# Kernel tuning notes

Measured on AMD Instinct MI355X. Metric: run time of the kernel, lower is better.

The kernel has to match this reference:

```python
import jax, jax.numpy as jnp
import numpy as np

N = 100000
E = 3200000
IN_C = 128
HID = 128


def setup_inputs() -> dict:
    key = jax.random.key(0)
    k1, k2, k3, k4, k5 = jax.random.split(key, 5)
    x = jax.random.normal(k1, (N, IN_C), dtype=jnp.float32)
    edge_index = jax.random.randint(k2, (2, E), 0, N, dtype=jnp.int64)
    edge_weight = jax.random.uniform(k3, (E,), dtype=jnp.float32)
    # GCNConv linear weight [out, in] (applied as x @ W.T), glorot-ish scale
    W = jax.random.normal(k4, (HID, IN_C), dtype=jnp.float32) / np.sqrt(IN_C)
    bias = jnp.zeros((HID,), dtype=jnp.float32)
    # PReLU per-channel alpha, torch default init 0.25
    alpha = jnp.full((HID,), 0.25, dtype=jnp.float32)
    return {"x": x, "edge_index": edge_index, "edge_weight": edge_weight,
            "W": W, "bias": bias, "alpha": alpha}


def reference(x, edge_index, edge_weight, W, bias, alpha):
    n = x.shape[0]
    # gcn_norm with self-loops (fill value 1.0)
    loop_idx = jnp.arange(n, dtype=edge_index.dtype)
    row = jnp.concatenate([edge_index[0], loop_idx])  # source
    col = jnp.concatenate([edge_index[1], loop_idx])  # target
    ew = jnp.concatenate([edge_weight, jnp.ones((n,), dtype=edge_weight.dtype)])
    deg = jax.ops.segment_sum(ew, col, num_segments=n)  # in-degree by weight
    dinv = jnp.where(deg > 0, jax.lax.rsqrt(deg), 0.0)
    norm = dinv[row] * ew * dinv[col]  # [E+N]
    # linear transform first (GCNConv order), then gather-scatter aggregation
    h = x @ W.T  # [N, HID]
    msgs = norm[:, None] * h[row]  # [E+N, HID]
    out = jax.ops.segment_sum(msgs, col, num_segments=n) + bias  # [N, HID]
    # PReLU with per-channel alpha
    return jnp.where(out > 0, out, alpha * out)
```

## Files before the change

### kernel.cpp

```cpp
#include <hip/hip_runtime.h>


#define NBLK    512
#define MAXBKT  1600
#define QSCALE  32767.0f

__device__ __forceinline__ unsigned bf16pack2(float a, float b) {
    unsigned ua = __float_as_uint(a);
    ua = (ua + 0x7fffu + ((ua >> 16) & 1u)) >> 16;
    unsigned ub = __float_as_uint(b);
    ub = (ub + 0x7fffu + ((ub >> 16) & 1u)) >> 16;
    return ua | (ub << 16);
}

__device__ __forceinline__ float2 bf16unpack2(unsigned u) {
    return make_float2(__uint_as_float(u << 16),
                       __uint_as_float(u & 0xffff0000u));
}

__global__ __launch_bounds__(256) void p1_hist(const int* __restrict__ col,
                                               unsigned* __restrict__ hist,
                                               int e, int nbkt, int epb) {
    __shared__ unsigned lh[MAXBKT];
    int b = blockIdx.x;
    for (int k = threadIdx.x; k < nbkt; k += 256) lh[k] = 0;
    __syncthreads();
    int s = b * epb, en = s + epb; if (en > e) en = e;
    for (int i = s + threadIdx.x; i < en; i += 256)
        atomicAdd(&lh[col[i] >> 6], 1u);
    __syncthreads();
    for (int k = threadIdx.x; k < nbkt; k += 256)
        hist[(size_t)k * NBLK + b] = lh[k];
}

__global__ __launch_bounds__(1024) void scan_partial2(
    const unsigned* __restrict__ a, unsigned* __restrict__ part, int m) {
    __shared__ unsigned red[1024];
    int t = threadIdx.x, i = blockIdx.x * 1024 + t;
    red[t] = (i < m) ? a[i] : 0;
    __syncthreads();
    #pragma unroll
    for (int d = 512; d > 0; d >>= 1) {
        if (t < d) red[t] += red[t + d];
        __syncthreads();
    }
    if (t == 0) part[blockIdx.x] = red[0];
}

__global__ __launch_bounds__(1024) void scan_base2(
    unsigned* __restrict__ part, int nb, int* __restrict__ offs, int n, int e) {
    __shared__ unsigned s[1024];
    int t = threadIdx.x;
    unsigned v = (t < nb) ? part[t] : 0;
    s[t] = v;
    __syncthreads();
    for (int d = 1; d < 1024; d <<= 1) {
        unsigned add = (t >= d) ? s[t - d] : 0;
        __syncthreads();
        s[t] += add;
        __syncthreads();
    }
    if (t < nb) part[t] = s[t] - v;
    if (t == 0) offs[n] = e;
}

__global__ __launch_bounds__(1024) void scan_write2(
    unsigned* __restrict__ a, const unsigned* __restrict__ part, int m) {
    __shared__ unsigned s[1024];
    int t = threadIdx.x, i = blockIdx.x * 1024 + t;
    unsigned v = (i < m) ? a[i] : 0;
    s[t] = v;
    __syncthreads();
    for (int d = 1; d < 1024; d <<= 1) {
        unsigned add = (t >= d) ? s[t - d] : 0;
        __syncthreads();
        s[t] += add;
        __syncthreads();
    }
    if (i < m) a[i] = part[blockIdx.x] + s[t] - v;
}

__global__ __launch_bounds__(256) void p2_scatter(
    const int* __restrict__ col, const int* __restrict__ row,
    const float* __restrict__ ew, const unsigned* __restrict__ base,
    unsigned long long* __restrict__ pay, int e, int nbkt, int epb) {
    __shared__ unsigned lbase[MAXBKT];
    __shared__ unsigned lcur[MAXBKT];
    int b = blockIdx.x;
    for (int k = threadIdx.x; k < nbkt; k += 256) {
        lbase[k] = base[(size_t)k * NBLK + b];
        lcur[k] = 0;
    }
    __syncthreads();
    int s = b * epb, en = s + epb; if (en > e) en = e;
    for (int i = s + threadIdx.x; i < en; i += 256) {
        int c = col[i];
        int bk = c >> 6;
        unsigned q  = (unsigned)(ew[i] * QSCALE + 0.5f);
        unsigned lo = ((unsigned)row[i] << 15) | q;
        unsigned rk = atomicAdd(&lcur[bk], 1u);
        pay[(size_t)lbase[bk] + rk] =
            ((unsigned long long)(unsigned)(c & 63) << 32) | lo;
    }
}

__global__ __launch_bounds__(256) void p3_build(
    const unsigned long long* __restrict__ pay,
    const unsigned* __restrict__ histBase,
    unsigned* __restrict__ csr, int* __restrict__ offs,
    float* __restrict__ dinv, int n, int nbkt, int e) {
    __shared__ unsigned cnt[64], wsum[64], lofs[64], cur[64];
    int bk = blockIdx.x;
    int zs = (int)histBase[(size_t)bk * NBLK];
    int ze = (bk + 1 < nbkt) ? (int)histBase[(size_t)(bk + 1) * NBLK] : e;
    int t = threadIdx.x;
    if (t < 64) { cnt[t] = 0; wsum[t] = 0; cur[t] = 0; }
    __syncthreads();
    for (int p = zs + t; p < ze; p += 256) {
        unsigned long long v = pay[p];
        int l = (int)(v >> 32) & 63;
        atomicAdd(&cnt[l], 1u);
        atomicAdd(&wsum[l], (unsigned)v & 0x7fffu);
    }
    __syncthreads();
    if (t == 0) {
        unsigned run = 0;
        for (int l = 0; l < 64; ++l) { lofs[l] = run; run += cnt[l]; }
    }
    __syncthreads();
    for (int p = zs + t; p < ze; p += 256) {
        unsigned long long v = pay[p];
        int l = (int)(v >> 32) & 63;
        unsigned rk = atomicAdd(&cur[l], 1u);
        csr[zs + lofs[l] + rk] = (unsigned)v;
    }
    if (t < 64) {
        int node = bk * 64 + t;
        if (node < n) {
            offs[node] = zs + (int)lofs[t];
            float dg = 1.0f + (float)wsum[t] * (1.0f / QSCALE);
            dinv[node] = rsqrtf(dg);
        }
    }
}

__global__ __launch_bounds__(256) void gemm_kernel(const float* __restrict__ x,
                                                   const float* __restrict__ W,
                                                   unsigned* __restrict__ h, int n) {
    __shared__ float Wt[128][128];
    int t = threadIdx.x;
    const float4* W4 = (const float4*)W;
    #pragma unroll
    for (int it = 0; it < 16; ++it) {
        int i = t + it * 256;
        float4 v = W4[i];
        int o  = i >> 5;
        int kb = (i & 31) << 2;
        Wt[kb + 0][o ^ (((kb + 0) & 7) << 2)] = v.x;
        Wt[kb + 1][o ^ (((kb + 1) & 7) << 2)] = v.y;
        Wt[kb + 2][o ^ (((kb + 2) & 7) << 2)] = v.z;
        Wt[kb + 3][o ^ (((kb + 3) & 7) << 2)] = v.w;
    }
    __syncthreads();

    int tc = t & 31;
    int rs = t >> 5;
    int r0 = blockIdx.x * 64 + rs * 8;
    if (r0 >= n) return;
    const float4* x4 = (const float4*)x;

    float acc[8][4];
    #pragma unroll
    for (int ri = 0; ri < 8; ++ri)
        #pragma unroll
        for (int j = 0; j < 4; ++j) acc[ri][j] = 0.0f;

    int rcnt = n - r0; if (rcnt > 8) rcnt = 8;

    if (rcnt == 8) {
        for (int kq = 0; kq < 32; ++kq) {
            int kb = kq << 2;
            float4 wv0 = *(const float4*)&Wt[kb + 0][(4 * tc) ^ (((kb + 0) & 7) << 2)];
            float4 wv1 = *(const float4*)&Wt[kb + 1][(4 * tc) ^ (((kb + 1) & 7) << 2)];
            float4 wv2 = *(const float4*)&Wt[kb + 2][(4 * tc) ^ (((kb + 2) & 7) << 2)];
            float4 wv3 = *(const float4*)&Wt[kb + 3][(4 * tc) ^ (((kb + 3) & 7) << 2)];
            #pragma unroll
            for (int ri = 0; ri < 8; ++ri) {
                float4 xv = x4[(size_t)(r0 + ri) * 32 + kq];
                acc[ri][0] += xv.x * wv0.x + xv.y * wv1.x + xv.z * wv2.x + xv.w * wv3.x;
                acc[ri][1] += xv.x * wv0.y + xv.y * wv1.y + xv.z * wv2.y + xv.w * wv3.y;
                acc[ri][2] += xv.x * wv0.z + xv.y * wv1.z + xv.z * wv2.z + xv.w * wv3.z;
                acc[ri][3] += xv.x * wv0.w + xv.y * wv1.w + xv.z * wv2.w + xv.w * wv3.w;
            }
        }
        uint2* h2 = (uint2*)h;
        #pragma unroll
        for (int ri = 0; ri < 8; ++ri)
            h2[(size_t)(r0 + ri) * 32 + tc] =
                make_uint2(bf16pack2(acc[ri][0], acc[ri][1]),
                           bf16pack2(acc[ri][2], acc[ri][3]));
    } else {
        for (int kq = 0; kq < 32; ++kq) {
            int kb = kq << 2;
            float4 wv0 = *(const float4*)&Wt[kb + 0][(4 * tc) ^ (((kb + 0) & 7) << 2)];
            float4 wv1 = *(const float4*)&Wt[kb + 1][(4 * tc) ^ (((kb + 1) & 7) << 2)];
            float4 wv2 = *(const float4*)&Wt[kb + 2][(4 * tc) ^ (((kb + 2) & 7) << 2)];
            float4 wv3 = *(const float4*)&Wt[kb + 3][(4 * tc) ^ (((kb + 3) & 7) << 2)];
            for (int ri = 0; ri < rcnt; ++ri) {
                float4 xv = x4[(size_t)(r0 + ri) * 32 + kq];
                acc[ri][0] += xv.x * wv0.x + xv.y * wv1.x + xv.z * wv2.x + xv.w * wv3.x;
                acc[ri][1] += xv.x * wv0.y + xv.y * wv1.y + xv.z * wv2.y + xv.w * wv3.y;
                acc[ri][2] += xv.x * wv0.z + xv.y * wv1.z + xv.z * wv2.z + xv.w * wv3.z;
                acc[ri][3] += xv.x * wv0.w + xv.y * wv1.w + xv.z * wv2.w + xv.w * wv3.w;
            }
        }
        uint2* h2 = (uint2*)h;
        for (int ri = 0; ri < rcnt; ++ri)
            h2[(size_t)(r0 + ri) * 32 + tc] =
                make_uint2(bf16pack2(acc[ri][0], acc[ri][1]),
                           bf16pack2(acc[ri][2], acc[ri][3]));
    }
}

__global__ __launch_bounds__(256) void aggregate_kernel(
    const unsigned* __restrict__ h, const unsigned* __restrict__ csr,
    const int* __restrict__ offs, const float* __restrict__ dinv,
    const float* __restrict__ bias, const float* __restrict__ alpha,
    float* __restrict__ out, int n) {
    int w = (blockIdx.x * 256 + threadIdx.x) >> 6;
    if (w >= n) return;
    int lane = threadIdx.x & 63;

    int beg = offs[w], end = offs[w + 1];
    float ax = 0.0f, ay = 0.0f;

    int i = beg;
    int end4 = beg + ((end - beg) & ~3);
    for (; i < end4; i += 4) {
        unsigned p0 = csr[i],     p1 = csr[i + 1];
        unsigned p2 = csr[i + 2], p3 = csr[i + 3];
        unsigned s0 = p0 >> 15, s1 = p1 >> 15, s2 = p2 >> 15, s3 = p3 >> 15;
        float d0 = dinv[s0], d1 = dinv[s1], d2 = dinv[s2], d3 = dinv[s3];
        float2 v0 = bf16unpack2(h[(size_t)s0 * 64 + lane]);
        float2 v1 = bf16unpack2(h[(size_t)s1 * 64 + lane]);
        float2 v2 = bf16unpack2(h[(size_t)s2 * 64 + lane]);
        float2 v3 = bf16unpack2(h[(size_t)s3 * 64 + lane]);
        float a0 = d0 * (float)(p0 & 0x7fffu) * (1.0f / QSCALE);
        float a1 = d1 * (float)(p1 & 0x7fffu) * (1.0f / QSCALE);
        float a2 = d2 * (float)(p2 & 0x7fffu) * (1.0f / QSCALE);
        float a3 = d3 * (float)(p3 & 0x7fffu) * (1.0f / QSCALE);
        ax += a0 * v0.x; ay += a0 * v0.y;
        ax += a1 * v1.x; ay += a1 * v1.y;
        ax += a2 * v2.x; ay += a2 * v2.y;
        ax += a3 * v3.x; ay += a3 * v3.y;
    }
    for (; i < end; ++i) {
        unsigned p = csr[i];
        unsigned s = p >> 15;
        float a = dinv[s] * (float)(p & 0x7fffu) * (1.0f / QSCALE);
        float2 v = bf16unpack2(h[(size_t)s * 64 + lane]);
        ax += a * v.x; ay += a * v.y;
    }

    float dc = dinv[w];
    float2 hc = bf16unpack2(h[(size_t)w * 64 + lane]);
    ax += dc * hc.x; ay += dc * hc.y;

    float2 bv = ((const float2*)bias)[lane];
    float2 av = ((const float2*)alpha)[lane];
    float ox = ax * dc + bv.x;
    float oy = ay * dc + bv.y;
    ox = ox > 0.0f ? ox : av.x * ox;
    oy = oy > 0.0f ? oy : av.y * oy;
    ((float2*)out)[(size_t)w * 64 + lane] = make_float2(ox, oy);
}

extern "C" void kernel_launch(void* const* d_in, const int* in_sizes, int n_in,
                              void* d_out, int out_size, void* d_ws, size_t ws_size,
                              hipStream_t stream) {
    const float* x     = (const float*)d_in[0];
    const int*   ei    = (const int*)d_in[1];
    const float* ew    = (const float*)d_in[2];
    const float* W     = (const float*)d_in[3];
    const float* bias  = (const float*)d_in[4];
    const float* alpha = (const float*)d_in[5];
    float* out = (float*)d_out;

    const int n = in_sizes[0] / 128;
    const int e = in_sizes[1] / 2;
    const int* row = ei;
    const int* col = ei + e;

    const int nbkt = (n + 63) >> 6;
    const int m    = nbkt * NBLK;
    const int epb  = (e + NBLK - 1) / NBLK;
    const int nb2  = (m + 1023) / 1024;

    char* ws = (char*)d_ws;
    size_t off = 0;
    auto alloc = [&](size_t bytes) -> char* {
        char* p = ws + off;
        off = (off + bytes + 255) & ~(size_t)255;
        return p;
    };
    unsigned*           hist = (unsigned*)          alloc((size_t)m * 4);
    unsigned*           part = (unsigned*)          alloc((size_t)1024 * 4);
    int*                offs = (int*)               alloc((size_t)(n + 1) * 4);
    float*              dinv = (float*)             alloc((size_t)n * 4);
    unsigned long long* pay  = (unsigned long long*)alloc((size_t)e * 8);
    unsigned*           csr  = (unsigned*)          alloc((size_t)e * 4);
    unsigned*           h    = (unsigned*)          alloc((size_t)n * 128 * 2);
    (void)ws_size; (void)n_in; (void)out_size;

    p1_hist<<<NBLK, 256, 0, stream>>>(col, hist, e, nbkt, epb);
    scan_partial2<<<nb2, 1024, 0, stream>>>(hist, part, m);
    scan_base2<<<1, 1024, 0, stream>>>(part, nb2, offs, n, e);
    scan_write2<<<nb2, 1024, 0, stream>>>(hist, part, m);
    p2_scatter<<<NBLK, 256, 0, stream>>>(col, row, ew, hist, pay, e, nbkt, epb);
    p3_build<<<nbkt, 256, 0, stream>>>(pay, hist, csr, offs, dinv, n, nbkt, e);

    int gg = (n + 63) / 64;
    gemm_kernel<<<gg, 256, 0, stream>>>(x, W, h, n);

    int ga = (n + 3) / 4;
    aggregate_kernel<<<ga, 256, 0, stream>>>(h, csr, offs, dinv, bias, alpha, out, n);
}
```

Baseline: 295.5 us.

## Precompute per-edge coefficients and swizzle aggregate block order across XCDs

Adds an af_fill kernel that computes each edge's normalized coefficient (dinv[src] times the dequantized weight) once into a float array, so the aggregate loop no longer performs a dependent random dinv gather per edge. The aggregate kernel also reads its row offsets through readfirstlane to keep them scalar, and remaps block IDs so consecutive node groups land on the same XCD when the grid is divisible by 8. The cost is an extra kernel launch plus a write and read of 4 bytes per edge. The swizzle only takes effect when the block count is a multiple of 8, which holds for n=100000.

```diff
diff --git a/kernel.cpp b/kernel.cpp
--- a/kernel.cpp
+++ b/kernel.cpp
@@ -141,6 +141,16 @@
             float dg = 1.0f + (float)wsum[t] * (1.0f / QSCALE);
             dinv[node] = rsqrtf(dg);
         }
+    }
+}
+
+__global__ __launch_bounds__(256) void af_fill(const unsigned* __restrict__ csr,
+                                               const float* __restrict__ dinv,
+                                               float* __restrict__ af, int e) {
+    int i = blockIdx.x * 256 + threadIdx.x;
+    if (i < e) {
+        unsigned v = csr[i];
+        af[i] = dinv[v >> 15] * ((float)(v & 0x7fffu) * (1.0f / QSCALE));
     }
 }
 
@@ -224,40 +234,40 @@
 
 __global__ __launch_bounds__(256) void aggregate_kernel(
     const unsigned* __restrict__ h, const unsigned* __restrict__ csr,
-    const int* __restrict__ offs, const float* __restrict__ dinv,
-    const float* __restrict__ bias, const float* __restrict__ alpha,
-    float* __restrict__ out, int n) {
-    int w = (blockIdx.x * 256 + threadIdx.x) >> 6;
+    const float* __restrict__ af, const int* __restrict__ offs,
+    const float* __restrict__ dinv, const float* __restrict__ bias,
+    const float* __restrict__ alpha, float* __restrict__ out, int n, int swzq) {
+    int bid = blockIdx.x;
+    int sb  = swzq ? ((bid & 7) * swzq + (bid >> 3)) : bid;
+    int w = sb * 4 + (threadIdx.x >> 6);
     if (w >= n) return;
     int lane = threadIdx.x & 63;
 
-    int beg = offs[w], end = offs[w + 1];
+    int beg = __builtin_amdgcn_readfirstlane(offs[w]);
+    int end = __builtin_amdgcn_readfirstlane(offs[w + 1]);
     float ax = 0.0f, ay = 0.0f;
 
     int i = beg;
     int end4 = beg + ((end - beg) & ~3);
     for (; i < end4; i += 4) {
-        unsigned p0 = csr[i],     p1 = csr[i + 1];
-        unsigned p2 = csr[i + 2], p3 = csr[i + 3];
-        unsigned s0 = p0 >> 15, s1 = p1 >> 15, s2 = p2 >> 15, s3 = p3 >> 15;
-        float d0 = dinv[s0], d1 = dinv[s1], d2 = dinv[s2], d3 = dinv[s3];
-        float2 v0 = bf16unpack2(h[(size_t)s0 * 64 + lane]);
-        float2 v1 = bf16unpack2(h[(size_t)s1 * 64 + lane]);
-        float2 v2 = bf16unpack2(h[(size_t)s2 * 64 + lane]);
-        float2 v3 = bf16unpack2(h[(size_t)s3 * 64 + lane]);
-        float a0 = d0 * (float)(p0 & 0x7fffu) * (1.0f / QSCALE);
-        float a1 = d1 * (float)(p1 & 0x7fffu) * (1.0f / QSCALE);
-        float a2 = d2 * (float)(p2 & 0x7fffu) * (1.0f / QSCALE);
-        float a3 = d3 * (float)(p3 & 0x7fffu) * (1.0f / QSCALE);
+        unsigned s0 = csr[i]     >> 15, s1 = csr[i + 1] >> 15;
+        unsigned s2 = csr[i + 2] >> 15, s3 = csr[i + 3] >> 15;
+        float a0 = af[i],     a1 = af[i + 1];
+        float a2 = af[i + 2], a3 = af[i + 3];
+        unsigned u0 = h[(size_t)s0 * 64 + lane];
+        unsigned u1 = h[(size_t)s1 * 64 + lane];
+        unsigned u2 = h[(size_t)s2 * 64 + lane];
+        unsigned u3 = h[(size_t)s3 * 64 + lane];
+        float2 v0 = bf16unpack2(u0), v1 = bf16unpack2(u1);
+        float2 v2 = bf16unpack2(u2), v3 = bf16unpack2(u3);
         ax += a0 * v0.x; ay += a0 * v0.y;
         ax += a1 * v1.x; ay += a1 * v1.y;
         ax += a2 * v2.x; ay += a2 * v2.y;
         ax += a3 * v3.x; ay += a3 * v3.y;
     }
     for (; i < end; ++i) {
-        unsigned p = csr[i];
-        unsigned s = p >> 15;
-        float a = dinv[s] * (float)(p & 0x7fffu) * (1.0f / QSCALE);
+        unsigned s = csr[i] >> 15;
+        float a = af[i];
         float2 v = bf16unpack2(h[(size_t)s * 64 + lane]);
         ax += a * v.x; ay += a * v.y;
     }
@@ -309,6 +319,7 @@
     float*              dinv = (float*)             alloc((size_t)n * 4);
     unsigned long long* pay  = (unsigned long long*)alloc((size_t)e * 8);
     unsigned*           csr  = (unsigned*)          alloc((size_t)e * 4);
+    float*              afv  = (float*)             alloc((size_t)e * 4);
     unsigned*           h    = (unsigned*)          alloc((size_t)n * 128 * 2);
     (void)ws_size; (void)n_in; (void)out_size;
 
@@ -318,10 +329,13 @@
     scan_write2<<<nb2, 1024, 0, stream>>>(hist, part, m);
     p2_scatter<<<NBLK, 256, 0, stream>>>(col, row, ew, hist, pay, e, nbkt, epb);
     p3_build<<<nbkt, 256, 0, stream>>>(pay, hist, csr, offs, dinv, n, nbkt, e);
+    af_fill<<<(e + 255) / 256, 256, 0, stream>>>(csr, dinv, afv, e);
 
     int gg = (n + 63) / 64;
     gemm_kernel<<<gg, 256, 0, stream>>>(x, W, h, n);
 
     int ga = (n + 3) / 4;
-    aggregate_kernel<<<ga, 256, 0, stream>>>(h, csr, offs, dinv, bias, alpha, out, n);
-}
+    int swzq = (ga % 8 == 0) ? ga / 8 : 0;
+    aggregate_kernel<<<ga, 256, 0, stream>>>(h, csr, afv, offs, dinv,
+                                             bias, alpha, out, n, swzq);
+}
```

Measured after the change: 296.1 us. Within noise of the previous version (+0.2%).

## Tile hidden features into column slabs and prefold source dinv into CSR weights

Applied to the files above, without the earlier changes.

The GEMM now writes h in a tiled layout: 8 slabs of 16 channels per node, so each 32-byte slab row belongs to one node. Aggregation runs over a 2D grid of node by slab. Each wave processes 8 edges at once, with 8 lanes covering 16 channels, then combines the partial sums with xor shuffles. A new pass folds dinv[src] into the quantized 15-bit edge weight, which removes the per-edge dinv gather but adds requantization error and an extra pass over the edges. The intent is to shrink each slab's gather footprint so it stays in cache, at the cost of reading the CSR eight times and doing more, narrower gathers.

```diff
diff --git a/kernel.cpp b/kernel.cpp
--- a/kernel.cpp
+++ b/kernel.cpp
@@ -4,6 +4,9 @@
 #define NBLK    512
 #define MAXBKT  1600
 #define QSCALE  32767.0f
+#define NTILE   8
+
+typedef float vfloat2 __attribute__((ext_vector_type(2)));
 
 __device__ __forceinline__ unsigned bf16pack2(float a, float b) {
     unsigned ua = __float_as_uint(a);
@@ -144,9 +147,20 @@
     }
 }
 
+__global__ __launch_bounds__(256) void csr2_fill(const unsigned* __restrict__ csr,
+                                                 const float* __restrict__ dinv,
+                                                 unsigned* __restrict__ csr2, int e) {
+    int i = blockIdx.x * 256 + threadIdx.x;
+    if (i < e) {
+        unsigned v = csr[i];
+        float a = dinv[v >> 15] * ((float)(v & 0x7fffu) * (1.0f / QSCALE));
+        csr2[i] = (v & 0xffff8000u) | (unsigned)(a * QSCALE + 0.5f);
+    }
+}
+
 __global__ __launch_bounds__(256) void gemm_kernel(const float* __restrict__ x,
                                                    const float* __restrict__ W,
-                                                   unsigned* __restrict__ h, int n) {
+                                                   unsigned* __restrict__ ht, int n) {
     __shared__ float Wt[128][128];
     int t = threadIdx.x;
     const float4* W4 = (const float4*)W;
@@ -176,6 +190,9 @@
         for (int j = 0; j < 4; ++j) acc[ri][j] = 0.0f;
 
     int rcnt = n - r0; if (rcnt > 8) rcnt = 8;
+
+    uint2* h2 = (uint2*)ht;
+    size_t obase = (size_t)(tc >> 2) * n * 4 + (tc & 3);
 
     if (rcnt == 8) {
         for (int kq = 0; kq < 32; ++kq) {
@@ -193,10 +210,9 @@
                 acc[ri][3] += xv.x * wv0.w + xv.y * wv1.w + xv.z * wv2.w + xv.w * wv3.w;
             }
         }
-        uint2* h2 = (uint2*)h;
         #pragma unroll
         for (int ri = 0; ri < 8; ++ri)
-            h2[(size_t)(r0 + ri) * 32 + tc] =
+            h2[obase + (size_t)(r0 + ri) * 4] =
                 make_uint2(bf16pack2(acc[ri][0], acc[ri][1]),
                            bf16pack2(acc[ri][2], acc[ri][3]));
     } else {
@@ -214,65 +230,67 @@
                 acc[ri][3] += xv.x * wv0.w + xv.y * wv1.w + xv.z * wv2.w + xv.w * wv3.w;
             }
         }
-        uint2* h2 = (uint2*)h;
         for (int ri = 0; ri < rcnt; ++ri)
-            h2[(size_t)(r0 + ri) * 32 + tc] =
+            h2[obase + (size_t)(r0 + ri) * 4] =
                 make_uint2(bf16pack2(acc[ri][0], acc[ri][1]),
                            bf16pack2(acc[ri][2], acc[ri][3]));
     }
 }
 
 __global__ __launch_bounds__(256) void aggregate_kernel(
-    const unsigned* __restrict__ h, const unsigned* __restrict__ csr,
+    const unsigned* __restrict__ ht, const unsigned* __restrict__ csr2,
     const int* __restrict__ offs, const float* __restrict__ dinv,
     const float* __restrict__ bias, const float* __restrict__ alpha,
     float* __restrict__ out, int n) {
-    int w = (blockIdx.x * 256 + threadIdx.x) >> 6;
+    int tile = blockIdx.y;
+    int w = blockIdx.x * 4 + (threadIdx.x >> 6);
     if (w >= n) return;
     int lane = threadIdx.x & 63;
-
-    int beg = offs[w], end = offs[w + 1];
+    int g = lane >> 3, c2 = lane & 7;
+    const unsigned* slab = ht + (size_t)tile * n * 8;
+
+    int beg = __builtin_amdgcn_readfirstlane(offs[w]);
+    int end = __builtin_amdgcn_readfirstlane(offs[w + 1]);
+
     float ax = 0.0f, ay = 0.0f;
-
-    int i = beg;
-    int end4 = beg + ((end - beg) & ~3);
-    for (; i < end4; i += 4) {
-        unsigned p0 = csr[i],     p1 = csr[i + 1];
-        unsigned p2 = csr[i + 2], p3 = csr[i + 3];
-        unsigned s0 = p0 >> 15, s1 = p1 >> 15, s2 = p2 >> 15, s3 = p3 >> 15;
-        float d0 = dinv[s0], d1 = dinv[s1], d2 = dinv[s2], d3 = dinv[s3];
-        float2 v0 = bf16unpack2(h[(size_t)s0 * 64 + lane]);
-        float2 v1 = bf16unpack2(h[(size_t)s1 * 64 + lane]);
-        float2 v2 = bf16unpack2(h[(size_t)s2 * 64 + lane]);
-        float2 v3 = bf16unpack2(h[(size_t)s3 * 64 + lane]);
-        float a0 = d0 * (float)(p0 & 0x7fffu) * (1.0f / QSCALE);
-        float a1 = d1 * (float)(p1 & 0x7fffu) * (1.0f / QSCALE);
-        float a2 = d2 * (float)(p2 & 0x7fffu) * (1.0f / QSCALE);
-        float a3 = d3 * (float)(p3 & 0x7fffu) * (1.0f / QSCALE);
-        ax += a0 * v0.x; ay += a0 * v0.y;
-        ax += a1 * v1.x; ay += a1 * v1.y;
-        ax += a2 * v2.x; ay += a2 * v2.y;
-        ax += a3 * v3.x; ay += a3 * v3.y;
-    }
-    for (; i < end; ++i) {
-        unsigned p = csr[i];
-        unsigned s = p >> 15;
-        float a = dinv[s] * (float)(p & 0x7fffu) * (1.0f / QSCALE);
-        float2 v = bf16unpack2(h[(size_t)s * 64 + lane]);
-        ax += a * v.x; ay += a * v.y;
-    }
-
-    float dc = dinv[w];
-    float2 hc = bf16unpack2(h[(size_t)w * 64 + lane]);
-    ax += dc * hc.x; ay += dc * hc.y;
-
-    float2 bv = ((const float2*)bias)[lane];
-    float2 av = ((const float2*)alpha)[lane];
-    float ox = ax * dc + bv.x;
-    float oy = ay * dc + bv.y;
-    ox = ox > 0.0f ? ox : av.x * ox;
-    oy = oy > 0.0f ? oy : av.y * oy;
-    ((float2*)out)[(size_t)w * 64 + lane] = make_float2(ox, oy);
+    int i = beg + g;
+    for (; i + 8 < end; i += 16) {
+        unsigned v0 = __builtin_nontemporal_load(&csr2[i]);
+        unsigned v1 = __builtin_nontemporal_load(&csr2[i + 8]);
+        unsigned u0 = slab[(size_t)(v0 >> 15) * 8 + c2];
+        unsigned u1 = slab[(size_t)(v1 >> 15) * 8 + c2];
+        float a0 = (float)(v0 & 0x7fffu) * (1.0f / QSCALE);
+        float a1 = (float)(v1 & 0x7fffu) * (1.0f / QSCALE);
+        float2 h0 = bf16unpack2(u0), h1 = bf16unpack2(u1);
+        ax += a0 * h0.x; ay += a0 * h0.y;
+        ax += a1 * h1.x; ay += a1 * h1.y;
+    }
+    if (i < end) {
+        unsigned v = __builtin_nontemporal_load(&csr2[i]);
+        unsigned u = slab[(size_t)(v >> 15) * 8 + c2];
+        float a = (float)(v & 0x7fffu) * (1.0f / QSCALE);
+        float2 hv = bf16unpack2(u);
+        ax += a * hv.x; ay += a * hv.y;
+    }
+
+    ax += __shfl_xor(ax, 8);  ay += __shfl_xor(ay, 8);
+    ax += __shfl_xor(ax, 16); ay += __shfl_xor(ay, 16);
+    ax += __shfl_xor(ax, 32); ay += __shfl_xor(ay, 32);
+
+    if (lane < 8) {
+        float dc = dinv[w];
+        float2 hw = bf16unpack2(slab[(size_t)w * 8 + lane]);
+        ax += dc * hw.x; ay += dc * hw.y;
+        float2 bv = ((const float2*)bias)[tile * 8 + lane];
+        float2 av = ((const float2*)alpha)[tile * 8 + lane];
+        float ox = ax * dc + bv.x;
+        float oy = ay * dc + bv.y;
+        ox = ox > 0.0f ? ox : av.x * ox;
+        oy = oy > 0.0f ? oy : av.y * oy;
+        vfloat2 ov; ov.x = ox; ov.y = oy;
+        __builtin_nontemporal_store(ov,
+            (vfloat2*)&((float2*)out)[(size_t)w * 64 + tile * 8 + lane]);
+    }
 }
 
 extern "C" void kernel_launch(void* const* d_in, const int* in_sizes, int n_in,
@@ -309,7 +327,8 @@
     float*              dinv = (float*)             alloc((size_t)n * 4);
     unsigned long long* pay  = (unsigned long long*)alloc((size_t)e * 8);
     unsigned*           csr  = (unsigned*)          alloc((size_t)e * 4);
-    unsigned*           h    = (unsigned*)          alloc((size_t)n * 128 * 2);
+    unsigned*           csr2 = (unsigned*)          alloc((size_t)e * 4);
+    unsigned*           ht   = (unsigned*)          alloc((size_t)n * 128 * 2);
     (void)ws_size; (void)n_in; (void)out_size;
 
     p1_hist<<<NBLK, 256, 0, stream>>>(col, hist, e, nbkt, epb);
@@ -318,10 +337,13 @@
     scan_write2<<<nb2, 1024, 0, stream>>>(hist, part, m);
     p2_scatter<<<NBLK, 256, 0, stream>>>(col, row, ew, hist, pay, e, nbkt, epb);
     p3_build<<<nbkt, 256, 0, stream>>>(pay, hist, csr, offs, dinv, n, nbkt, e);
+    csr2_fill<<<(e + 255) / 256, 256, 0, stream>>>(csr, dinv, csr2, e);
 
     int gg = (n + 63) / 64;
-    gemm_kernel<<<gg, 256, 0, stream>>>(x, W, h, n);
+    gemm_kernel<<<gg, 256, 0, stream>>>(x, W, ht, n);
 
     int ga = (n + 3) / 4;
-    aggregate_kernel<<<ga, 256, 0, stream>>>(h, csr, offs, dinv, bias, alpha, out, n);
-}
+    dim3 grid(ga, NTILE);
+    aggregate_kernel<<<grid, 256, 0, stream>>>(ht, csr2, offs, dinv,
+                                               bias, alpha, out, n);
+}
```

New measurement: 566.6 us. 1.92x slower.
